# Performance work log

Measured on AMD Instinct MI355X. Metric: run time of the kernel, lower is better.

The kernel has to match this reference:

```python
import jax, jax.numpy as jnp
import numpy as np

H, B, C, T, F = 4, 2, 64, 2048, 64   # n_head, batch, in_chan, time, n_freqs
HID = 4                               # hid_chan (per-head Q/K channels)
VD = C // H                           # per-head V channels
EPS = 1e-5


def prelu(x, a):
    return jnp.where(x >= 0, x, a * x)


def ln_cf(x, g, b):
    # LayerNormalization4D: normalize over (channel, freq) axes of (..., C, T, F)
    mu = x.mean(axis=(-3, -1), keepdims=True)
    var = ((x - mu) ** 2).mean(axis=(-3, -1), keepdims=True)
    return (x - mu) / jnp.sqrt(var + EPS) * g + b


def setup_inputs() -> dict:
    key = jax.random.key(0)
    ks = jax.random.split(key, 8)

    def w(k, shape):
        return jax.random.normal(k, shape, jnp.float32) * 0.05

    return {
        "x": jax.random.normal(ks[0], (B, C, T, F), jnp.float32),
        # per-head 1x1-conv Q/K/V projections (stacked over head axis)
        "Wq": w(ks[1], (H, HID, C)), "bq": jnp.zeros((H, HID), jnp.float32),
        "aq": jnp.full((H,), 0.25, jnp.float32),
        "gq": jnp.ones((H, HID, F), jnp.float32), "betq": jnp.zeros((H, HID, F), jnp.float32),
        "Wk": w(ks[2], (H, HID, C)), "bk": jnp.zeros((H, HID), jnp.float32),
        "ak": jnp.full((H,), 0.25, jnp.float32),
        "gk": jnp.ones((H, HID, F), jnp.float32), "betk": jnp.zeros((H, HID, F), jnp.float32),
        "Wv": w(ks[3], (H, VD, C)), "bv": jnp.zeros((H, VD), jnp.float32),
        "av": jnp.full((H,), 0.25, jnp.float32),
        "gv": jnp.ones((H, VD, F), jnp.float32), "betv": jnp.zeros((H, VD, F), jnp.float32),
        # output 1x1-conv projection
        "Wp": w(ks[4], (C, C)), "bp": jnp.zeros((C,), jnp.float32),
        "ap": jnp.full((), 0.25, jnp.float32),
        "gp": jnp.ones((C, F), jnp.float32), "betp": jnp.zeros((C, F), jnp.float32),
    }


def reference(x, Wq, bq, aq, gq, betq, Wk, bk, ak, gk, betk,
              Wv, bv, av, gv, betv, Wp, bp, ap, gp, betp):
    def qkv(W, b, a, g, be):
        # batched per-head 1x1 conv: (H,O,C) x (B,C,T,F) -> (H,B,O,T,F)
        y = jnp.einsum('hoc,bctf->hbotf', W, x) + b[:, None, :, None, None]
        y = prelu(y, a[:, None, None, None, None])
        return ln_cf(y, g[:, None, :, None, :], be[:, None, :, None, :])

    Q = qkv(Wq, bq, aq, gq, betq).reshape(H * B, HID, T, F)
    K = qkv(Wk, bk, ak, gk, betk).reshape(H * B, HID, T, F)
    V = qkv(Wv, bv, av, gv, betv).reshape(H * B, VD, T, F)

    # (HB, C', T, F) -> (HB, T, C'*F)
    Q = Q.transpose(0, 2, 1, 3).reshape(H * B, T, HID * F)
    K = K.transpose(0, 2, 1, 3).reshape(H * B, T, HID * F)
    V = V.transpose(0, 2, 1, 3).reshape(H * B, T, VD * F)

    scale = 1.0 / jnp.sqrt(jnp.asarray(HID * F, jnp.float32))
    attn = jax.nn.softmax(jnp.einsum('bqd,bkd->bqk', Q, K) * scale, axis=-1)  # (HB,T,T)
    O = jnp.einsum('bqk,bkd->bqd', attn, V)                                    # (HB,T,VD*F)

    # (HB,T,VD,F) -> (B, H*VD, T, F) matching torch head-concat order
    O = O.reshape(H * B, T, VD, F).transpose(0, 2, 1, 3)
    O = O.reshape(H, B, VD, T, F).transpose(1, 0, 2, 3, 4).reshape(B, H * VD, T, F)

    y = jnp.einsum('oc,bctf->botf', Wp, O) + bp[None, :, None, None]
    y = prelu(y, ap)
    y = ln_cf(y, gp[:, None, :], betp[:, None, :])
    return y + x
```

## Files before the change

### kernel.cpp

```cpp
#include <hip/hip_runtime.h>

#define EPS_ 1e-5f

typedef float f32x4 __attribute__((ext_vector_type(4)));
typedef short s16x8 __attribute__((ext_vector_type(8)));

static __device__ __forceinline__ short f2bf(float f) {
    unsigned u = __float_as_uint(f);
    unsigned r = (u + 0x7FFFu + ((u >> 16) & 1u)) >> 16;
    return (short)r;
}
static __device__ __forceinline__ float bf2f(short s) {
    return __uint_as_float(((unsigned)(unsigned short)s) << 16);
}

static __device__ __forceinline__ void gload16(const short* g, short* l) {
    __builtin_amdgcn_global_load_lds(
        (const __attribute__((address_space(1))) unsigned int*)g,
        (__attribute__((address_space(3))) unsigned int*)l, 16, 0, 0);
}

__global__ __launch_bounds__(256) void prep_kernel(
    const float* __restrict__ Wq, const float* __restrict__ Wk,
    const float* __restrict__ Wv, const float* __restrict__ Wp,
    short* __restrict__ Wbf, short* __restrict__ Wpbf)
{
    int i = blockIdx.x * 256 + threadIdx.x;
    if (i < 6144) {
        float v = (i < 1024) ? Wq[i] : (i < 2048 ? Wk[i - 1024] : Wv[i - 2048]);
        Wbf[i] = f2bf(v);
    } else if (i < 6144 + 4096) {
        Wpbf[i - 6144] = f2bf(Wp[i - 6144]);
    }
}

__global__ __launch_bounds__(256) void qkv_kernel(
    const float* __restrict__ x, const short* __restrict__ Wbf,
    const float* __restrict__ bq, const float* __restrict__ aq,
    const float* __restrict__ gq, const float* __restrict__ betq,
    const float* __restrict__ bk, const float* __restrict__ ak,
    const float* __restrict__ gk, const float* __restrict__ betk,
    const float* __restrict__ bv, const float* __restrict__ av,
    const float* __restrict__ gv, const float* __restrict__ betv,
    short* __restrict__ Qo, short* __restrict__ Ko, short* __restrict__ Vo)
{
    const int t = blockIdx.x;
    const int b = blockIdx.y;
    const int tid = threadIdx.x;
    const int wid = tid >> 6, lane = tid & 63;
    const int g = lane >> 4, c16 = lane & 15;
    const int f_ = tid & 63, cg = tid >> 6;

    __shared__ __align__(16) short wlds[96 * 64];
    __shared__ __align__(16) short xs[64 * 64];
    __shared__ float zs[96 * 64];
    __shared__ float stats[12][2];
    __shared__ float bias_l[96], alpha_l[96];

#pragma unroll
    for (int j = 0; j < 3; ++j) {
        int i8 = tid + 256 * j;
        int row = i8 >> 3, cb = i8 & 7;
        s16x8 v = *(const s16x8*)(Wbf + i8 * 8);
        *(s16x8*)&wlds[row * 64 + ((cb ^ (row & 7)) * 8)] = v;
    }
    if (tid < 96) {
        int row = tid; float bias, al;
        if (row < 16)      { bias = bq[row];      al = aq[row >> 2]; }
        else if (row < 32) { bias = bk[row - 16]; al = ak[(row - 16) >> 2]; }
        else               { bias = bv[row - 32]; al = av[(row - 32) >> 4]; }
        bias_l[row] = bias; alpha_l[row] = al;
    }
#pragma unroll
    for (int it = 0; it < 2; ++it) {
        int cb = cg + 4 * it, c0 = cb * 8;
        s16x8 v;
#pragma unroll
        for (int i = 0; i < 8; ++i)
            v[i] = f2bf(x[(((size_t)b * 64 + c0 + i) * 2048 + t) * 64 + f_]);
        *(s16x8*)&xs[f_ * 64 + ((cb ^ (f_ & 7)) * 8)] = v;
    }
    __syncthreads();

    const int f0 = wid * 16;
    s16x8 bfr[2];
#pragma unroll
    for (int kk = 0; kk < 2; ++kk)
        bfr[kk] = *(const s16x8*)&xs[(f0 + c16) * 64 + (((kk * 4 + g) ^ (c16 & 7)) * 8)];

    f32x4 acc[6];
#pragma unroll
    for (int rt = 0; rt < 6; ++rt) {
#pragma unroll
        for (int r = 0; r < 4; ++r) acc[rt][r] = 0.f;
#pragma unroll
        for (int kk = 0; kk < 2; ++kk) {
            s16x8 a = *(const s16x8*)&wlds[(rt * 16 + c16) * 64 + (((kk * 4 + g) ^ (c16 & 7)) * 8)];
            acc[rt] = __builtin_amdgcn_mfma_f32_16x16x32_bf16(a, bfr[kk], acc[rt], 0, 0, 0);
        }
    }

#pragma unroll
    for (int rt = 0; rt < 6; ++rt)
#pragma unroll
        for (int r = 0; r < 4; ++r) {
            int row = rt * 16 + g * 4 + r;
            float z = acc[rt][r] + bias_l[row];
            z = z >= 0.f ? z : alpha_l[row] * z;
            zs[row * 64 + f0 + c16] = z;
        }
    __syncthreads();

#pragma unroll
    for (int gi = 0; gi < 3; ++gi) {
        int grp = wid * 3 + gi;
        int base_row, n;
        if (grp < 4)      { base_row = grp * 4;             n = 256; }
        else if (grp < 8) { base_row = 16 + (grp - 4) * 4;  n = 256; }
        else              { base_row = 32 + (grp - 8) * 16; n = 1024; }
        int cnt = n >> 6;
        float s = 0.f, ss = 0.f;
        for (int i = 0; i < cnt; ++i) {
            float v = zs[(base_row + i) * 64 + lane];
            s += v; ss += v * v;
        }
#pragma unroll
        for (int msk = 32; msk >= 1; msk >>= 1) {
            s  += __shfl_xor(s, msk);
            ss += __shfl_xor(ss, msk);
        }
        if (lane == 0) {
            float mean = s / n;
            float var = ss / n - mean * mean;
            stats[grp][0] = mean;
            stats[grp][1] = rsqrtf(var + EPS_);
        }
    }
    __syncthreads();

#pragma unroll
    for (int j = 0; j < 24; ++j) {
        int row = cg + 4 * j;
        float zv = zs[row * 64 + f_];
        if (row < 16) {
            int grp = row >> 2;
            float val = (zv - stats[grp][0]) * stats[grp][1];
            val = val * gq[row * 64 + f_] + betq[row * 64 + f_];
            int h = row >> 2, o = row & 3;
            Qo[(((size_t)(h * 2 + b)) * 2048 + t) * 256 + o * 64 + f_] = f2bf(val);
        } else if (row < 32) {
            int rr = row - 16, grp = 4 + (rr >> 2);
            float val = (zv - stats[grp][0]) * stats[grp][1];
            val = val * gk[rr * 64 + f_] + betk[rr * 64 + f_];
            int h = rr >> 2, o = rr & 3;
            Ko[(((size_t)(h * 2 + b)) * 2048 + t) * 256 + o * 64 + f_] = f2bf(val);
        } else {
            int rr = row - 32, grp = 8 + (rr >> 4);
            float val = (zv - stats[grp][0]) * stats[grp][1];
            val = val * gv[rr * 64 + f_] + betv[rr * 64 + f_];
            int h = rr >> 4, ov = rr & 15;
            Vo[(((size_t)(h * 2 + b)) * 2048 + t) * 1024 + ov * 64 + f_] = f2bf(val);
        }
    }
}

__global__ __launch_bounds__(256) void vtrans_kernel(
    const short* __restrict__ Vrm, short* __restrict__ Vt)
{
    const int t0 = blockIdx.x * 64;
    const int d0 = blockIdx.y * 64;
    const int hb = blockIdx.z;
    const int tid = threadIdx.x;
    __shared__ __align__(16) short tile[64 * 72];

#pragma unroll
    for (int k = 0; k < 2; ++k) {
        int q = tid + 256 * k;
        int row = q >> 3, slot = q & 7;
        s16x8 v = *(const s16x8*)(Vrm + ((size_t)hb * 2048 + t0 + row) * 1024 + d0 + slot * 8);
        *(s16x8*)&tile[row * 72 + slot * 8] = v;
    }
    __syncthreads();
#pragma unroll
    for (int k = 0; k < 2; ++k) {
        int q = tid + 256 * k;
        int drow = q >> 3, tslot = q & 7;
        s16x8 v;
#pragma unroll
        for (int i = 0; i < 8; ++i) {
            int c = tslot * 8 + i;
            int cl = c & 31;
            int src = (c & 32) + ((cl >> 2) & 1) * 16 + ((cl >> 4) & 1) * 8
                    + ((cl >> 3) & 1) * 4 + (cl & 3);
            v[i] = tile[src * 72 + drow];
        }
        *(s16x8*)(Vt + ((size_t)hb * 1024 + d0 + drow) * 2048 + t0 + tslot * 8) = v;
    }
}

__global__ __launch_bounds__(512, 2) void attn_kernel(
    const short* __restrict__ Qg, const short* __restrict__ Kg,
    const short* __restrict__ Vt, short* __restrict__ Ob)
{
    const int hb = blockIdx.x;
    const int qt = blockIdx.y;
    const int dh = blockIdx.z;
    const int t0 = qt * 128;
    const int tid = threadIdx.x;
    const int lane = tid & 63;
    const int wid = tid >> 6;
    const int g = lane >> 4, c16 = lane & 15;

    __shared__ __align__(16) short k_lds[4][32 * 256];
    __shared__ __align__(16) short v_lds[2][512 * 32];
    __shared__ __align__(16) short p_lds[2][8][512];
    __shared__ float l_sh[128];

    const size_t kgbase = (size_t)hb * 2048 * 256;
    const size_t vgbase = ((size_t)hb * 1024 + dh * 512) * 2048;
    const int dsl = wid * 64;

    const size_t qrow = (size_t)hb * 2048 + t0 + wid * 16 + c16;
    s16x8 qf[8];
#pragma unroll
    for (int kf = 0; kf < 8; ++kf)
        qf[kf] = *(const s16x8*)(Qg + qrow * 256 + kf * 32 + g * 8);

    f32x4 oacc[32];
#pragma unroll
    for (int i = 0; i < 32; ++i)
#pragma unroll
        for (int r = 0; r < 4; ++r) oacc[i][r] = 0.f;

    float l_r = 0.f;

#define STAGE_K(buf, kt) do {                                                  \
    _Pragma("unroll")                                                          \
    for (int j_ = 0; j_ < 2; ++j_) {                                           \
        int c_ = tid + 512 * j_;                                               \
        int row_ = c_ >> 5, sp_ = c_ & 31;                                     \
        int sl_ = sp_ ^ (row_ & 7);                                            \
        gload16(Kg + kgbase + (size_t)((kt) * 32 + row_) * 256 + sl_ * 8,      \
                &k_lds[buf][c_ * 8]);                                          \
    }                                                                          \
} while (0)

#define STAGE_V(buf, kt) do {                                                  \
    _Pragma("unroll")                                                          \
    for (int j_ = 0; j_ < 4; ++j_) {                                           \
        int c_ = tid + 512 * j_;                                               \
        int row_ = c_ >> 2, sp_ = c_ & 3;                                      \
        int sl_ = sp_ ^ ((row_ >> 1) & 3);                                     \
        gload16(Vt + vgbase + (size_t)row_ * 2048 + (kt) * 32 + sl_ * 8,       \
                &v_lds[buf][c_ * 8]);                                          \
    }                                                                          \
} while (0)

#define QKT_PHASE(nt) do {                                                     \
    f32x4 sf0, sf1;                                                            \
    _Pragma("unroll")                                                          \
    for (int r = 0; r < 4; ++r) { sf0[r] = 0.f; sf1[r] = 0.f; }                \
    __builtin_amdgcn_s_setprio(1);                                             \
    _Pragma("unroll")                                                          \
    for (int kf = 0; kf < 8; ++kf) {                                           \
        int sl_ = ((kf * 4 + g) ^ (c16 & 7)) * 8;                              \
        s16x8 ka0 = *(const s16x8*)&k_lds[(nt) & 3][c16 * 256 + sl_];          \
        sf0 = __builtin_amdgcn_mfma_f32_16x16x32_bf16(ka0, qf[kf], sf0, 0, 0, 0); \
        s16x8 ka1 = *(const s16x8*)&k_lds[(nt) & 3][(16 + c16) * 256 + sl_];   \
        sf1 = __builtin_amdgcn_mfma_f32_16x16x32_bf16(ka1, qf[kf], sf1, 0, 0, 0); \
    }                                                                          \
    __builtin_amdgcn_s_setprio(0);                                             \
    float rs = 0.f;                                                            \
    _Pragma("unroll")                                                          \
    for (int r = 0; r < 4; ++r) {                                              \
        float p0 = __expf(sf0[r] * 0.0625f);                                   \
        float p1 = __expf(sf1[r] * 0.0625f);                                   \
        sf0[r] = p0; sf1[r] = p1;                                              \
        rs += p0 + p1;                                                         \
    }                                                                          \
    rs += __shfl_xor(rs, 16);                                                  \
    rs += __shfl_xor(rs, 32);                                                  \
    l_r += rs;                                                                 \
    s16x8 pa;                                                                  \
    _Pragma("unroll")                                                          \
    for (int e = 0; e < 8; ++e)                                                \
        pa[e] = f2bf((e & 4) ? sf1[e & 3] : sf0[e & 3]);                       \
    *(s16x8*)&p_lds[(nt) & 1][wid][lane * 8] = pa;                             \
} while (0)

#define TILE_BARRIER4() do {                                                   \
    __builtin_amdgcn_sched_barrier(0);                                         \
    asm volatile("s_waitcnt vmcnt(4) lgkmcnt(0)" ::: "memory");                \
    __builtin_amdgcn_sched_barrier(0);                                         \
    __builtin_amdgcn_s_barrier();                                              \
} while (0)
#define TILE_BARRIER0() do {                                                   \
    __builtin_amdgcn_sched_barrier(0);                                         \
    asm volatile("s_waitcnt vmcnt(0) lgkmcnt(0)" ::: "memory");                \
    __builtin_amdgcn_sched_barrier(0);                                         \
    __builtin_amdgcn_s_barrier();                                              \
} while (0)

    STAGE_K(0, 0);
    STAGE_K(1, 1);
    STAGE_V(0, 0);
    __syncthreads();
    STAGE_K(2, 2);
    QKT_PHASE(0);
    __builtin_amdgcn_sched_barrier(0);
    asm volatile("s_waitcnt vmcnt(4) lgkmcnt(0)" ::: "memory");
    __builtin_amdgcn_sched_barrier(0);
    __builtin_amdgcn_s_barrier();

    for (int t = 0; t < 64; ++t) {
        const int buf = t & 1;

        if (t < 63) STAGE_V(buf ^ 1, t + 1);
        if (t < 61) STAGE_K((t + 3) & 3, t + 3);
        if (t < 63) QKT_PHASE(t + 1);

        s16x8 vb[4];
#pragma unroll
        for (int dt = 0; dt < 4; ++dt) {
            int rowv = dsl + dt * 16 + c16;
            vb[dt] = *(const s16x8*)&v_lds[buf][rowv * 32 + ((g ^ ((c16 >> 1) & 3)) * 8)];
        }
        __builtin_amdgcn_s_setprio(1);
#pragma unroll
        for (int qs = 0; qs < 8; ++qs) {
            s16x8 pa = *(const s16x8*)&p_lds[buf][qs][lane * 8];
#pragma unroll
            for (int dt = 0; dt < 4; ++dt)
                oacc[qs * 4 + dt] = __builtin_amdgcn_mfma_f32_16x16x32_bf16(
                    pa, vb[dt], oacc[qs * 4 + dt], 0, 0, 0);
        }
        __builtin_amdgcn_s_setprio(0);

        if (t < 61)      TILE_BARRIER4();
        else if (t < 63) TILE_BARRIER0();
    }

#undef STAGE_K
#undef STAGE_V
#undef QKT_PHASE
#undef TILE_BARRIER4
#undef TILE_BARRIER0

    __syncthreads();
    if (lane < 16) l_sh[wid * 16 + lane] = l_r;
    __syncthreads();

    const int h = hb >> 1, b = hb & 1;
#pragma unroll
    for (int qs = 0; qs < 8; ++qs) {
        float li[4];
#pragma unroll
        for (int r = 0; r < 4; ++r)
            li[r] = 1.f / l_sh[qs * 16 + g * 4 + r];
#pragma unroll
        for (int dt = 0; dt < 4; ++dt) {
            int vcol = dh * 512 + dsl + dt * 16 + c16;
            int cout = h * 16 + (vcol >> 6), ff = vcol & 63;
#pragma unroll
            for (int r = 0; r < 4; ++r) {
                int trow = t0 + qs * 16 + g * 4 + r;
                Ob[(((size_t)b * 64 + cout) * 2048 + trow) * 64 + ff] =
                    f2bf(oacc[qs * 4 + dt][r] * li[r]);
            }
        }
    }
}

__global__ __launch_bounds__(256) void oproj_kernel(
    const short* __restrict__ Ob, const float* __restrict__ x,
    const short* __restrict__ Wpbf,
    const float* __restrict__ bp, const float* __restrict__ ap,
    const float* __restrict__ gp, const float* __restrict__ betp,
    float* __restrict__ out)
{
    const int t = blockIdx.x;
    const int b = blockIdx.y;
    const int tid = threadIdx.x;
    const int wid = tid >> 6, lane = tid & 63;
    const int g = lane >> 4, c16 = lane & 15;
    const int f_ = tid & 63, cg = tid >> 6;

    __shared__ __align__(16) short wp[64 * 64];
    __shared__ __align__(16) short os[64 * 64];
    __shared__ float zs[64 * 64];
    __shared__ float red[4][2];

#pragma unroll
    for (int j = 0; j < 2; ++j) {
        int i8 = tid + 256 * j;
        int row = i8 >> 3, cb = i8 & 7;
        s16x8 v = *(const s16x8*)(Wpbf + i8 * 8);
        *(s16x8*)&wp[row * 64 + ((cb ^ (row & 7)) * 8)] = v;
    }
#pragma unroll
    for (int it = 0; it < 2; ++it) {
        int cb = cg + 4 * it, c0 = cb * 8;
        s16x8 v;
#pragma unroll
        for (int i = 0; i < 8; ++i)
            v[i] = Ob[(((size_t)b * 64 + c0 + i) * 2048 + t) * 64 + f_];
        *(s16x8*)&os[f_ * 64 + ((cb ^ (f_ & 7)) * 8)] = v;
    }
    __syncthreads();

    const int f0 = wid * 16;
    s16x8 bfr[2];
#pragma unroll
    for (int kk = 0; kk < 2; ++kk)
        bfr[kk] = *(const s16x8*)&os[(f0 + c16) * 64 + (((kk * 4 + g) ^ (c16 & 7)) * 8)];

    const float ap0 = ap[0];
    f32x4 acc[4];
#pragma unroll
    for (int rt = 0; rt < 4; ++rt) {
#pragma unroll
        for (int r = 0; r < 4; ++r) acc[rt][r] = 0.f;
#pragma unroll
        for (int kk = 0; kk < 2; ++kk) {
            s16x8 a = *(const s16x8*)&wp[(rt * 16 + c16) * 64 + (((kk * 4 + g) ^ (c16 & 7)) * 8)];
            acc[rt] = __builtin_amdgcn_mfma_f32_16x16x32_bf16(a, bfr[kk], acc[rt], 0, 0, 0);
        }
    }

#pragma unroll
    for (int rt = 0; rt < 4; ++rt)
#pragma unroll
        for (int r = 0; r < 4; ++r) {
            int row = rt * 16 + g * 4 + r;
            float z = acc[rt][r] + bp[row];
            z = z >= 0.f ? z : ap0 * z;
            zs[row * 64 + f0 + c16] = z;
        }
    __syncthreads();

    float s = 0.f, ss = 0.f;
#pragma unroll
    for (int j = 0; j < 16; ++j) {
        float v = zs[(cg + 4 * j) * 64 + f_];
        s += v; ss += v * v;
    }
#pragma unroll
    for (int msk = 32; msk >= 1; msk >>= 1) {
        s  += __shfl_xor(s, msk);
        ss += __shfl_xor(ss, msk);
    }
    if (lane == 0) { red[wid][0] = s; red[wid][1] = ss; }
    __syncthreads();
    float ts  = red[0][0] + red[1][0] + red[2][0] + red[3][0];
    float tss = red[0][1] + red[1][1] + red[2][1] + red[3][1];
    float mean = ts * (1.f / 4096.f);
    float rstd = rsqrtf(tss * (1.f / 4096.f) - mean * mean + EPS_);

#pragma unroll
    for (int j = 0; j < 16; ++j) {
        int row = cg + 4 * j;
        size_t idx = (((size_t)b * 64 + row) * 2048 + t) * 64 + f_;
        out[idx] = (zs[row * 64 + f_] - mean) * rstd * gp[row * 64 + f_]
                 + betp[row * 64 + f_] + x[idx];
    }
}

extern "C" void kernel_launch(void* const* d_in, const int* in_sizes, int n_in,
                              void* d_out, int out_size, void* d_ws, size_t ws_size,
                              hipStream_t stream)
{
    const float* x    = (const float*)d_in[0];
    const float* Wq   = (const float*)d_in[1];
    const float* bq   = (const float*)d_in[2];
    const float* aq   = (const float*)d_in[3];
    const float* gq   = (const float*)d_in[4];
    const float* betq = (const float*)d_in[5];
    const float* Wk   = (const float*)d_in[6];
    const float* bk   = (const float*)d_in[7];
    const float* ak   = (const float*)d_in[8];
    const float* gk   = (const float*)d_in[9];
    const float* betk = (const float*)d_in[10];
    const float* Wv   = (const float*)d_in[11];
    const float* bv   = (const float*)d_in[12];
    const float* av   = (const float*)d_in[13];
    const float* gv   = (const float*)d_in[14];
    const float* betv = (const float*)d_in[15];
    const float* Wp   = (const float*)d_in[16];
    const float* bp   = (const float*)d_in[17];
    const float* ap   = (const float*)d_in[18];
    const float* gp   = (const float*)d_in[19];
    const float* betp = (const float*)d_in[20];

    short* Qb   = (short*)d_ws;
    short* Kb   = Qb   + (size_t)8 * 2048 * 256;
    short* Vrm  = Kb   + (size_t)8 * 2048 * 256;
    short* Vt   = Vrm  + (size_t)8 * 2048 * 1024;
    short* Obuf = Vt   + (size_t)8 * 2048 * 1024;
    short* Wbf  = Obuf + (size_t)8 * 2048 * 1024;
    short* Wpbf = Wbf  + 96 * 64;

    prep_kernel<<<40, 256, 0, stream>>>(Wq, Wk, Wv, Wp, Wbf, Wpbf);
    qkv_kernel<<<dim3(2048, 2), 256, 0, stream>>>(x, Wbf,
        bq, aq, gq, betq, bk, ak, gk, betk, bv, av, gv, betv, Qb, Kb, Vrm);
    vtrans_kernel<<<dim3(32, 16, 8), 256, 0, stream>>>(Vrm, Vt);
    attn_kernel<<<dim3(8, 16, 2), 512, 0, stream>>>(Qb, Kb, Vt, Obuf);
    oproj_kernel<<<dim3(2048, 2), 256, 0, stream>>>(Obuf, x, Wpbf,
        bp, ap, gp, betp, (float*)d_out);
}
```

Before: 235.2 us.

## Fuse weight bf16 conversion into kernels and repartition QK^T work across waves

Removes the separate prep kernel and converts the Q/K/V and projection weights to bf16 inside the qkv and oproj kernels, saving a launch at the cost of redundant conversion per block. In attention, each wave now computes scores for 32 query rows against half of the 32-key tile, sharing each K fragment across two MFMAs. This reduces LDS K reads per wave but doubles Q fragment registers. Row sums are combined from two wave halves through shared memory, and the pipeline wait count is adjusted.

```diff
diff --git a/kernel.cpp b/kernel.cpp
--- a/kernel.cpp
+++ b/kernel.cpp
@@ -3,6 +3,7 @@
 #define EPS_ 1e-5f
 
 typedef float f32x4 __attribute__((ext_vector_type(4)));
+typedef short s16x4 __attribute__((ext_vector_type(4)));
 typedef short s16x8 __attribute__((ext_vector_type(8)));
 
 static __device__ __forceinline__ short f2bf(float f) {
@@ -20,22 +21,10 @@
         (__attribute__((address_space(3))) unsigned int*)l, 16, 0, 0);
 }
 
-__global__ __launch_bounds__(256) void prep_kernel(
+__global__ __launch_bounds__(256) void qkv_kernel(
+    const float* __restrict__ x,
     const float* __restrict__ Wq, const float* __restrict__ Wk,
-    const float* __restrict__ Wv, const float* __restrict__ Wp,
-    short* __restrict__ Wbf, short* __restrict__ Wpbf)
-{
-    int i = blockIdx.x * 256 + threadIdx.x;
-    if (i < 6144) {
-        float v = (i < 1024) ? Wq[i] : (i < 2048 ? Wk[i - 1024] : Wv[i - 2048]);
-        Wbf[i] = f2bf(v);
-    } else if (i < 6144 + 4096) {
-        Wpbf[i - 6144] = f2bf(Wp[i - 6144]);
-    }
-}
-
-__global__ __launch_bounds__(256) void qkv_kernel(
-    const float* __restrict__ x, const short* __restrict__ Wbf,
+    const float* __restrict__ Wv,
     const float* __restrict__ bq, const float* __restrict__ aq,
     const float* __restrict__ gq, const float* __restrict__ betq,
     const float* __restrict__ bk, const float* __restrict__ ak,
@@ -61,7 +50,14 @@
     for (int j = 0; j < 3; ++j) {
         int i8 = tid + 256 * j;
         int row = i8 >> 3, cb = i8 & 7;
-        s16x8 v = *(const s16x8*)(Wbf + i8 * 8);
+        int idx = i8 * 8;
+        const float* src = (idx < 1024) ? (Wq + idx)
+                         : (idx < 2048) ? (Wk + idx - 1024) : (Wv + idx - 2048);
+        f32x4 a0 = *(const f32x4*)src;
+        f32x4 a1 = *(const f32x4*)(src + 4);
+        s16x8 v;
+#pragma unroll
+        for (int i = 0; i < 4; ++i) { v[i] = f2bf(a0[i]); v[4 + i] = f2bf(a1[i]); }
         *(s16x8*)&wlds[row * 64 + ((cb ^ (row & 7)) * 8)] = v;
     }
     if (tid < 96) {
@@ -209,22 +205,26 @@
     const int tid = threadIdx.x;
     const int lane = tid & 63;
     const int wid = tid >> 6;
+    const int qs2 = wid >> 1;
+    const int kp = wid & 1;
     const int g = lane >> 4, c16 = lane & 15;
 
     __shared__ __align__(16) short k_lds[4][32 * 256];
     __shared__ __align__(16) short v_lds[2][512 * 32];
     __shared__ __align__(16) short p_lds[2][8][512];
-    __shared__ float l_sh[128];
+    __shared__ float l_sh[2][128];
 
     const size_t kgbase = (size_t)hb * 2048 * 256;
     const size_t vgbase = ((size_t)hb * 1024 + dh * 512) * 2048;
     const int dsl = wid * 64;
 
-    const size_t qrow = (size_t)hb * 2048 + t0 + wid * 16 + c16;
-    s16x8 qf[8];
-#pragma unroll
-    for (int kf = 0; kf < 8; ++kf)
-        qf[kf] = *(const s16x8*)(Qg + qrow * 256 + kf * 32 + g * 8);
+    const size_t qrowA = (size_t)hb * 2048 + t0 + qs2 * 32 + c16;
+    s16x8 qfA[8], qfB[8];
+#pragma unroll
+    for (int kf = 0; kf < 8; ++kf) {
+        qfA[kf] = *(const s16x8*)(Qg + qrowA * 256 + kf * 32 + g * 8);
+        qfB[kf] = *(const s16x8*)(Qg + (qrowA + 16) * 256 + kf * 32 + g * 8);
+    }
 
     f32x4 oacc[32];
 #pragma unroll
@@ -232,7 +232,7 @@
 #pragma unroll
         for (int r = 0; r < 4; ++r) oacc[i][r] = 0.f;
 
-    float l_r = 0.f;
+    float l_rA = 0.f, l_rB = 0.f;
 
 #define STAGE_K(buf, kt) do {                                                  \
     _Pragma("unroll")                                                          \
@@ -257,40 +257,39 @@
 } while (0)
 
 #define QKT_PHASE(nt) do {                                                     \
-    f32x4 sf0, sf1;                                                            \
+    f32x4 sfA, sfB;                                                            \
     _Pragma("unroll")                                                          \
-    for (int r = 0; r < 4; ++r) { sf0[r] = 0.f; sf1[r] = 0.f; }                \
+    for (int r = 0; r < 4; ++r) { sfA[r] = 0.f; sfB[r] = 0.f; }                \
     __builtin_amdgcn_s_setprio(1);                                             \
     _Pragma("unroll")                                                          \
     for (int kf = 0; kf < 8; ++kf) {                                           \
         int sl_ = ((kf * 4 + g) ^ (c16 & 7)) * 8;                              \
-        s16x8 ka0 = *(const s16x8*)&k_lds[(nt) & 3][c16 * 256 + sl_];          \
-        sf0 = __builtin_amdgcn_mfma_f32_16x16x32_bf16(ka0, qf[kf], sf0, 0, 0, 0); \
-        s16x8 ka1 = *(const s16x8*)&k_lds[(nt) & 3][(16 + c16) * 256 + sl_];   \
-        sf1 = __builtin_amdgcn_mfma_f32_16x16x32_bf16(ka1, qf[kf], sf1, 0, 0, 0); \
+        s16x8 ka = *(const s16x8*)&k_lds[(nt) & 3][(kp * 16 + c16) * 256 + sl_]; \
+        sfA = __builtin_amdgcn_mfma_f32_16x16x32_bf16(ka, qfA[kf], sfA, 0, 0, 0); \
+        sfB = __builtin_amdgcn_mfma_f32_16x16x32_bf16(ka, qfB[kf], sfB, 0, 0, 0); \
     }                                                                          \
     __builtin_amdgcn_s_setprio(0);                                             \
-    float rs = 0.f;                                                            \
+    float rsA = 0.f, rsB = 0.f;                                                \
     _Pragma("unroll")                                                          \
     for (int r = 0; r < 4; ++r) {                                              \
-        float p0 = __expf(sf0[r] * 0.0625f);                                   \
-        float p1 = __expf(sf1[r] * 0.0625f);                                   \
-        sf0[r] = p0; sf1[r] = p1;                                              \
-        rs += p0 + p1;                                                         \
+        float pA = __expf(sfA[r] * 0.0625f);                                   \
+        float pB = __expf(sfB[r] * 0.0625f);                                   \
+        sfA[r] = pA; sfB[r] = pB;                                              \
+        rsA += pA; rsB += pB;                                                  \
     }                                                                          \
-    rs += __shfl_xor(rs, 16);                                                  \
-    rs += __shfl_xor(rs, 32);                                                  \
-    l_r += rs;                                                                 \
-    s16x8 pa;                                                                  \
+    rsA += __shfl_xor(rsA, 16); rsA += __shfl_xor(rsA, 32);                    \
+    rsB += __shfl_xor(rsB, 16); rsB += __shfl_xor(rsB, 32);                    \
+    l_rA += rsA; l_rB += rsB;                                                  \
+    s16x4 pkA, pkB;                                                            \
     _Pragma("unroll")                                                          \
-    for (int e = 0; e < 8; ++e)                                                \
-        pa[e] = f2bf((e & 4) ? sf1[e & 3] : sf0[e & 3]);                       \
-    *(s16x8*)&p_lds[(nt) & 1][wid][lane * 8] = pa;                             \
+    for (int r = 0; r < 4; ++r) { pkA[r] = f2bf(sfA[r]); pkB[r] = f2bf(sfB[r]); } \
+    *(s16x4*)&p_lds[(nt) & 1][qs2 * 2][lane * 8 + kp * 4] = pkA;               \
+    *(s16x4*)&p_lds[(nt) & 1][qs2 * 2 + 1][lane * 8 + kp * 4] = pkB;           \
 } while (0)
 
-#define TILE_BARRIER4() do {                                                   \
+#define TILE_BARRIER2() do {                                                   \
     __builtin_amdgcn_sched_barrier(0);                                         \
-    asm volatile("s_waitcnt vmcnt(4) lgkmcnt(0)" ::: "memory");                \
+    asm volatile("s_waitcnt vmcnt(2) lgkmcnt(0)" ::: "memory");                \
     __builtin_amdgcn_sched_barrier(0);                                         \
     __builtin_amdgcn_s_barrier();                                              \
 } while (0)
@@ -307,10 +306,7 @@
     __syncthreads();
     STAGE_K(2, 2);
     QKT_PHASE(0);
-    __builtin_amdgcn_sched_barrier(0);
-    asm volatile("s_waitcnt vmcnt(4) lgkmcnt(0)" ::: "memory");
-    __builtin_amdgcn_sched_barrier(0);
-    __builtin_amdgcn_s_barrier();
+    TILE_BARRIER2();
 
     for (int t = 0; t < 64; ++t) {
         const int buf = t & 1;
@@ -336,18 +332,21 @@
         }
         __builtin_amdgcn_s_setprio(0);
 
-        if (t < 61)      TILE_BARRIER4();
+        if (t < 61)      TILE_BARRIER2();
         else if (t < 63) TILE_BARRIER0();
     }
 
 #undef STAGE_K
 #undef STAGE_V
 #undef QKT_PHASE
-#undef TILE_BARRIER4
+#undef TILE_BARRIER2
 #undef TILE_BARRIER0
 
     __syncthreads();
-    if (lane < 16) l_sh[wid * 16 + lane] = l_r;
+    if (lane < 16) {
+        l_sh[kp][qs2 * 32 + lane] = l_rA;
+        l_sh[kp][qs2 * 32 + 16 + lane] = l_rB;
+    }
     __syncthreads();
 
     const int h = hb >> 1, b = hb & 1;
@@ -355,8 +354,10 @@
     for (int qs = 0; qs < 8; ++qs) {
         float li[4];
 #pragma unroll
-        for (int r = 0; r < 4; ++r)
-            li[r] = 1.f / l_sh[qs * 16 + g * 4 + r];
+        for (int r = 0; r < 4; ++r) {
+            int row = qs * 16 + g * 4 + r;
+            li[r] = 1.f / (l_sh[0][row] + l_sh[1][row]);
+        }
 #pragma unroll
         for (int dt = 0; dt < 4; ++dt) {
             int vcol = dh * 512 + dsl + dt * 16 + c16;
@@ -373,7 +374,7 @@
 
 __global__ __launch_bounds__(256) void oproj_kernel(
     const short* __restrict__ Ob, const float* __restrict__ x,
-    const short* __restrict__ Wpbf,
+    const float* __restrict__ Wp,
     const float* __restrict__ bp, const float* __restrict__ ap,
     const float* __restrict__ gp, const float* __restrict__ betp,
     float* __restrict__ out)
@@ -394,7 +395,11 @@
     for (int j = 0; j < 2; ++j) {
         int i8 = tid + 256 * j;
         int row = i8 >> 3, cb = i8 & 7;
-        s16x8 v = *(const s16x8*)(Wpbf + i8 * 8);
+        f32x4 a0 = *(const f32x4*)(Wp + i8 * 8);
+        f32x4 a1 = *(const f32x4*)(Wp + i8 * 8 + 4);
+        s16x8 v;
+#pragma unroll
+        for (int i = 0; i < 4; ++i) { v[i] = f2bf(a0[i]); v[4 + i] = f2bf(a1[i]); }
         *(s16x8*)&wp[row * 64 + ((cb ^ (row & 7)) * 8)] = v;
     }
 #pragma unroll
@@ -496,14 +501,11 @@
     short* Vrm  = Kb   + (size_t)8 * 2048 * 256;
     short* Vt   = Vrm  + (size_t)8 * 2048 * 1024;
     short* Obuf = Vt   + (size_t)8 * 2048 * 1024;
-    short* Wbf  = Obuf + (size_t)8 * 2048 * 1024;
-    short* Wpbf = Wbf  + 96 * 64;
-
-    prep_kernel<<<40, 256, 0, stream>>>(Wq, Wk, Wv, Wp, Wbf, Wpbf);
-    qkv_kernel<<<dim3(2048, 2), 256, 0, stream>>>(x, Wbf,
+
+    qkv_kernel<<<dim3(2048, 2), 256, 0, stream>>>(x, Wq, Wk, Wv,
         bq, aq, gq, betq, bk, ak, gk, betk, bv, av, gv, betv, Qb, Kb, Vrm);
     vtrans_kernel<<<dim3(32, 16, 8), 256, 0, stream>>>(Vrm, Vt);
     attn_kernel<<<dim3(8, 16, 2), 512, 0, stream>>>(Qb, Kb, Vt, Obuf);
-    oproj_kernel<<<dim3(2048, 2), 256, 0, stream>>>(Obuf, x, Wpbf,
+    oproj_kernel<<<dim3(2048, 2), 256, 0, stream>>>(Obuf, x, Wp,
         bp, ap, gp, betp, (float*)d_out);
 }
```

After: 233.7 us, median of 2. About the same (-0.6%).
